# Optimization experiments

Hardware: AMD Instinct MI355X
Metric: run time of the kernel (lower is better)

The kernel has to match this reference:

```python
import jax, jax.numpy as jnp
import numpy as np

TOP_K = 15
TEMPERATURE = 1.0
NEG_SLOPE = 0.2


def setup_inputs() -> dict:
    key = jax.random.key(0)
    ks = jax.random.split(key, 6)
    N, H, heads, hd = 4096, 256, 4, 64
    E_c = 131072
    embeddings = jax.random.normal(ks[0], (N, H), dtype=jnp.float32)
    # nn.Linear(H, heads*hd, bias=False) weight: [heads*hd, H], xavier-ish scale
    W = jax.random.normal(ks[1], (heads * hd, H), dtype=jnp.float32) * (1.0 / np.sqrt(H))
    att = jax.random.normal(ks[2], (heads, 2 * hd), dtype=jnp.float32) * 0.1
    corr_lambda = jnp.ones((1,), dtype=jnp.float32)
    sector_mask = jax.random.uniform(ks[3], (N, N)) > 0.05
    active_mask = jnp.ones((N,), dtype=bool)
    corr_edge_index = jax.random.randint(ks[4], (2, E_c), 0, N)
    corr_edge_weight = jax.random.uniform(ks[5], (E_c,), minval=-1.0, maxval=1.0)
    return dict(embeddings=embeddings, W=W, att=att, corr_lambda=corr_lambda,
                sector_mask=sector_mask, active_mask=active_mask,
                corr_edge_index=corr_edge_index, corr_edge_weight=corr_edge_weight)


def reference(embeddings, W, att, corr_lambda, sector_mask, active_mask,
              corr_edge_index, corr_edge_weight):
    N = embeddings.shape[0]
    heads = att.shape[0]
    hd = att.shape[1] // 2
    # h: [N, heads, hd]
    h = (embeddings @ W.T).reshape(N, heads, hd)
    # algebraic split of concat([h_i || h_j]) . att  ->  s_dst[i] + s_src[j]
    a_dst, a_src = att[:, :hd], att[:, hd:]
    s_dst = jnp.einsum('nhd,hd->nh', h, a_dst)  # coefficient of row node i
    s_src = jnp.einsum('nhd,hd->nh', h, a_src)  # coefficient of col node j
    # [N, N, heads] broadcast-add, leaky_relu, mean over heads
    scores = jax.nn.leaky_relu(s_dst[:, None, :] + s_src[None, :, :], NEG_SLOPE)
    scores = scores.mean(axis=-1) / TEMPERATURE  # [N, N]
    mask = (active_mask[:, None] & active_mask[None, :]) & sector_mask  # [N, N]
    scores = jnp.where(mask, scores, -jnp.inf)
    # correlation prior scattered into a dense matrix (index-assign semantics)
    corr = jnp.zeros((N, N), dtype=scores.dtype).at[
        corr_edge_index[0], corr_edge_index[1]].set(corr_edge_weight.astype(scores.dtype))
    corr = corr * mask.astype(scores.dtype)
    scores = scores + corr_lambda[0] * corr
    k = min(TOP_K, N - 1)
    topk_scores, topk_idx = jax.lax.top_k(scores, k)  # per-row top-k over src dim
    rows = jnp.broadcast_to(jnp.arange(N)[:, None], (N, k))
    # dense mask guarantees all top-k entries are finite -> E = N*k fixed
    edge_index = jnp.stack([topk_idx.reshape(-1), rows.reshape(-1)], axis=0)  # [2, N*k]
    edge_weight = jax.nn.softmax(topk_scores, axis=1).reshape(-1)  # [N*k]
    return edge_index, edge_weight
```

## Files before the change

kernel.cpp:

```cpp
#include <hip/hip_runtime.h>
#include <math.h>

#define H_DIM 256
#define HEADS 4
#define HD 64
#define TOPK 15
#define NSLOPE 0.2
#define NSLOPEF 0.2f
#define EDGE_CAP_MAX 128
#define CAND_CAP 256

__global__ __launch_bounds__(256) void prep1_kernel(const float* __restrict__ W,
                                                    const float* __restrict__ att,
                                                    double* __restrict__ wa_dst,
                                                    double* __restrict__ wa_src,
                                                    int* __restrict__ cnt,
                                                    unsigned int* __restrict__ abits,
                                                    const int* __restrict__ active) {
    const int b = blockIdx.x;
    cnt[b * 256 + threadIdx.x] = 0;
    if (b < 2 * HEADS) {
        const int k = threadIdx.x;
        const int h = b >> 1;
        const int side = b & 1;
        double a = 0.0;
        for (int d = 0; d < HD; ++d)
            a += (double)W[(h * HD + d) * H_DIM + k] * (double)att[h * 2 * HD + side * HD + d];
        (side ? wa_src : wa_dst)[h * H_DIM + k] = a;
    } else if (b == 8 && threadIdx.x < 128) {
        const int* ap = active + threadIdx.x * 32;
        unsigned int wv = 0;
        for (int t = 0; t < 32; ++t)
            if (ap[t]) wv |= 1u << t;
        abits[threadIdx.x] = wv;
    }
}

__global__ __launch_bounds__(256) void prep2_kernel(
    const float* __restrict__ emb, const double* __restrict__ wa_dst,
    const double* __restrict__ wa_src, double* __restrict__ s_dst,
    double* __restrict__ s_src, float* __restrict__ s_dst_f,
    float* __restrict__ s_src_f, const int* __restrict__ eidx,
    const float* __restrict__ ew, int* __restrict__ cnt,
    int4* __restrict__ etab, int N, int E, int cap) {
    const int b = blockIdx.x;
    const int tid = threadIdx.x;

    if (b < 1024) {
        const int lane = tid & 63;
        const int wid = tid >> 6;
        const int i = b * 4 + wid;
        double e[4];
#pragma unroll
        for (int m = 0; m < 4; ++m) e[m] = (double)emb[(size_t)i * H_DIM + lane + 64 * m];
        double acc[8];
#pragma unroll
        for (int c = 0; c < 8; ++c) {
            const double* wa = (c & 1) ? wa_src : wa_dst;
            const int h = c >> 1;
            double a = 0.0;
#pragma unroll
            for (int m = 0; m < 4; ++m) a += e[m] * wa[h * H_DIM + lane + 64 * m];
            acc[c] = a;
        }
#pragma unroll
        for (int m = 1; m < 64; m <<= 1) {
#pragma unroll
            for (int c = 0; c < 8; ++c) acc[c] += __shfl_xor(acc[c], m, 64);
        }
        if (lane == 0) {
#pragma unroll
            for (int c = 0; c < 8; ++c) {
                const int h = c >> 1;
                if (c & 1) {
                    s_src[i * HEADS + h] = acc[c];
                    s_src_f[i * HEADS + h] = (float)acc[c];
                } else {
                    s_dst[i * HEADS + h] = acc[c];
                    s_dst_f[i * HEADS + h] = (float)acc[c];
                }
            }
        }
    } else {
        const int e = (b - 1024) * 256 + tid;
        if (e < E) {
            const int r = eidx[e];
            const int c = eidx[E + e];
            const int s = atomicAdd(&cnt[r], 1);
            if (s < cap) {
                int4 rec;
                rec.x = c;
                rec.y = e;
                rec.z = __float_as_int(ew[e]);
                rec.w = 0;
                etab[r * cap + s] = rec;
            }
        }
    }
}

#define FOR16(OP) OP(0) OP(1) OP(2) OP(3) OP(4) OP(5) OP(6) OP(7) \
                  OP(8) OP(9) OP(10) OP(11) OP(12) OP(13) OP(14) OP(15)

__global__ __launch_bounds__(256) void main_kernel(
    const double* __restrict__ s_dst, const double* __restrict__ s_src,
    const float* __restrict__ s_dst_f, const float* __restrict__ s_src_f,
    const int* __restrict__ sector_mask, const unsigned short* __restrict__ abits16,
    const int* __restrict__ active, const float* __restrict__ lam_p,
    const int* __restrict__ cnt, const int4* __restrict__ etab,
    float* __restrict__ out, int N, int cap) {
    const int i = blockIdx.x;
    const int tid = threadIdx.x;
    const int lane = tid & 63;
    const int wid = tid >> 6;

    __shared__ int ec[EDGE_CAP_MAX];
    __shared__ int ee[EDGE_CAP_MAX];
    __shared__ float ewl[EDGE_CAP_MAX];
    __shared__ int wcol[EDGE_CAP_MAX];
    __shared__ double wadd[EDGE_CAP_MAX];
    __shared__ unsigned int wth[4];
    __shared__ double cand_v[CAND_CAP];
    __shared__ int cand_i[CAND_CAP];
    __shared__ int cand_cnt, wcnt;
    __shared__ double sorted_v[TOPK];
    __shared__ int sorted_i[TOPK];
    __shared__ double exps[TOPK];

    if (tid == 0) { cand_cnt = 0; wcnt = 0; }

    int deg = cnt[i];
    if (deg > cap) deg = cap;
    for (int p = tid; p < deg; p += 256) {
        const int4 rec = etab[i * cap + p];
        ec[p] = rec.x;
        ee[p] = rec.y;
        ewl[p] = __int_as_float(rec.z);
    }
    __syncthreads();

    const int* mrow = sector_mask + (size_t)i * N;
    const int4 m0 = *(const int4*)(mrow + 16 * tid);
    const int4 m1 = *(const int4*)(mrow + 16 * tid + 4);
    const int4 m2 = *(const int4*)(mrow + 16 * tid + 8);
    const int4 m3 = *(const int4*)(mrow + 16 * tid + 12);
    const unsigned int act_us = (unsigned int)abits16[tid];
    unsigned int pb = 0;
#define PB(C, VAL) if ((VAL) != 0) pb |= (1u << (C));
    PB(0, m0.x)  PB(1, m0.y)  PB(2, m0.z)  PB(3, m0.w)
    PB(4, m1.x)  PB(5, m1.y)  PB(6, m1.z)  PB(7, m1.w)
    PB(8, m2.x)  PB(9, m2.y)  PB(10, m2.z) PB(11, m2.w)
    PB(12, m3.x) PB(13, m3.y) PB(14, m3.z) PB(15, m3.w)
#undef PB
    pb &= act_us;

    const int lhi = lane >> 4;
    const int llo = lane & 15;
    unsigned int pm = 0;
#pragma unroll
    for (int k = 0; k < 16; ++k) {
        const unsigned int opb = (unsigned int)__shfl((int)pb, 4 * k + lhi, 64);
        pm |= ((opb >> llo) & 1u) << k;
    }
    if (active[i] == 0) pm = 0;

    const float sdf0 = s_dst_f[i * 4 + 0];
    const float sdf1 = s_dst_f[i * 4 + 1];
    const float sdf2 = s_dst_f[i * 4 + 2];
    const float sdf3 = s_dst_f[i * 4 + 3];
    const double sd0 = s_dst[i * 4 + 0];
    const double sd1 = s_dst[i * 4 + 1];
    const double sd2 = s_dst[i * 4 + 2];
    const double sd3 = s_dst[i * 4 + 3];
    const double lam = (double)lam_p[0];
    const double4* __restrict__ s_src4 = (const double4*)s_src;
    const float4* __restrict__ s_srcf4 = (const float4*)s_src_f;
    const int jbase = (wid << 10) | lane;

    float f0, f1, f2, f3, f4, f5, f6, f7, f8, f9, f10, f11, f12, f13, f14, f15;
#define INIT_SLOT(K) { \
    const bool m = (pm >> K) & 1u; \
    const float4 sv = s_srcf4[jbase + (K << 6)]; \
    float x0 = sdf0 + sv.x, x1 = sdf1 + sv.y, x2 = sdf2 + sv.z, x3 = sdf3 + sv.w; \
    x0 = (x0 < 0.0f) ? NSLOPEF * x0 : x0; \
    x1 = (x1 < 0.0f) ? NSLOPEF * x1 : x1; \
    x2 = (x2 < 0.0f) ? NSLOPEF * x2 : x2; \
    x3 = (x3 < 0.0f) ? NSLOPEF * x3 : x3; \
    f##K = m ? (0.25f * (x0 + x1 + x2 + x3)) : -INFINITY; }
    FOR16(INIT_SLOT)
#undef INIT_SLOT

    if (tid < deg) {
        const int c = ec[tid];
        const int eid = ee[tid];
        bool win = true;
        for (int q = 0; q < deg; ++q)
            if (ec[q] == c && ee[q] > eid) win = false;
        if (win) {
            int p = atomicAdd(&wcnt, 1);
            wcol[p] = c;
            wadd[p] = lam * (double)ewl[tid];
        }
    }
    __syncthreads();

    const int nw = wcnt;
    for (int w = 0; w < nw; ++w) {
        const int c = wcol[w];
        if ((((c >> 10) << 6) | (c & 63)) == tid) {
            const float addf = (float)wadd[w];
            const int kk = (c >> 6) & 15;
#define ADD_SLOT(K) if (kk == K) f##K += addf;
            FOR16(ADD_SLOT)
#undef ADD_SLOT
        }
    }

    unsigned int k0, k1, k2, k3, k4, k5, k6, k7, k8, k9, k10, k11, k12, k13, k14, k15;
#define KEY_SLOT(K) { const unsigned u = __float_as_uint(f##K); \
    k##K = u ^ ((unsigned)((int)u >> 31) | 0x80000000u); }
    FOR16(KEY_SLOT)
#undef KEY_SLOT
    unsigned int lmax = k0;
#define LMAX(K) if (k##K > lmax) lmax = k##K;
    FOR16(LMAX)
#undef LMAX

    unsigned int th = 0;
    for (int b = 31; b >= 0; --b) {
        const unsigned int trial = th | (1u << b);
        unsigned long long m = __ballot(lmax >= trial);
        if (__popcll(m) >= TOPK) th = trial;
    }
    if (lane == 0) wth[wid] = th;
    __syncthreads();
    th = wth[0];
    if (wth[1] > th) th = wth[1];
    if (wth[2] > th) th = wth[2];
    if (wth[3] > th) th = wth[3];
    th = (th > 256u) ? (th - 256u) : 0u;

#define FILT(K) if (k##K >= th) { int p = atomicAdd(&cand_cnt, 1); \
    if (p < CAND_CAP) cand_i[p] = jbase + (K << 6); }
    FOR16(FILT)
#undef FILT
    __syncthreads();

    int C = cand_cnt;
    if (C > CAND_CAP) C = CAND_CAP;
    if (tid < C) {
        const int j = cand_i[tid];
        const double4 sv = s_src4[j];
        double x0 = sd0 + sv.x, x1 = sd1 + sv.y, x2 = sd2 + sv.z, x3 = sd3 + sv.w;
        x0 = (x0 < 0.0) ? NSLOPE * x0 : x0;
        x1 = (x1 < 0.0) ? NSLOPE * x1 : x1;
        x2 = (x2 < 0.0) ? NSLOPE * x2 : x2;
        x3 = (x3 < 0.0) ? NSLOPE * x3 : x3;
        double v = 0.25 * (x0 + x1 + x2 + x3);
        for (int w = 0; w < nw; ++w)
            if (wcol[w] == j) v += wadd[w];
        cand_v[tid] = v;
    }
    __syncthreads();

    if (tid < C) {
        const double mv = cand_v[tid];
        const int mi = cand_i[tid];
        int rank = 0;
        for (int q = 0; q < C; ++q) {
            const double qv = cand_v[q];
            const int qi = cand_i[q];
            rank += ((qv > mv) || (qv == mv && qi < mi)) ? 1 : 0;
        }
        if (rank < TOPK) { sorted_v[rank] = mv; sorted_i[rank] = mi; }
    }
    __syncthreads();

    if (tid < TOPK) exps[tid] = exp(sorted_v[tid] - sorted_v[0]);
    __syncthreads();
    if (tid < TOPK) {
        double s = 0.0;
        for (int t = 0; t < TOPK; ++t) s += exps[t];
        const int NK = N * TOPK;
        const int base = i * TOPK + tid;
        out[base] = (float)sorted_i[tid];
        out[NK + base] = (float)i;
        out[2 * NK + base] = (float)(exps[tid] / s);
    }
}

extern "C" void kernel_launch(void* const* d_in, const int* in_sizes, int n_in,
                              void* d_out, int out_size, void* d_ws, size_t ws_size,
                              hipStream_t stream) {
    const float* emb    = (const float*)d_in[0];
    const float* W      = (const float*)d_in[1];
    const float* att    = (const float*)d_in[2];
    const float* lam    = (const float*)d_in[3];
    const int*   sector = (const int*)d_in[4];
    const int*   active = (const int*)d_in[5];
    const int*   eidx   = (const int*)d_in[6];
    const float* ew     = (const float*)d_in[7];
    float* out = (float*)d_out;

    const int N = in_sizes[5];
    const int E = in_sizes[6] / 2;

    double* wa_dst = (double*)d_ws;
    double* wa_src = wa_dst + HEADS * H_DIM;
    double* s_dst  = wa_src + HEADS * H_DIM;
    double* s_src  = s_dst + (size_t)N * HEADS;
    float* s_dst_f = (float*)(s_src + (size_t)N * HEADS);
    float* s_src_f = s_dst_f + (size_t)N * HEADS;
    int* cnt       = (int*)(s_src_f + (size_t)N * HEADS);
    unsigned int* abits = (unsigned int*)(cnt + N);
    uintptr_t ep = (uintptr_t)(abits + N / 32);
    ep = (ep + 15) & ~(uintptr_t)15;
    int4* etab = (int4*)ep;

    size_t used = (ep - (uintptr_t)d_ws) + 64;
    size_t rem = (ws_size > used) ? (ws_size - used) : 0;
    int cap = (int)(rem / ((size_t)N * 16));
    if (cap > EDGE_CAP_MAX) cap = EDGE_CAP_MAX;
    if (cap < 16) cap = 16;

    const int nb = (E + 255) / 256;

    prep1_kernel<<<16, 256, 0, stream>>>(W, att, wa_dst, wa_src, cnt, abits, active);
    prep2_kernel<<<1024 + nb, 256, 0, stream>>>(emb, wa_dst, wa_src, s_dst, s_src,
                                                s_dst_f, s_src_f, eidx, ew, cnt,
                                                etab, N, E, cap);
    main_kernel<<<N, 256, 0, stream>>>(s_dst, s_src, s_dst_f, s_src_f, sector,
                                       (const unsigned short*)abits, active, lam, cnt,
                                       etab, out, N, cap);
}
```

Baseline: 179.6 us.

## Tile s_dst/s_src projection through shared memory, 16 rows per block

```diff
diff --git a/kernel.cpp b/kernel.cpp
--- a/kernel.cpp
+++ b/kernel.cpp
@@ -9,6 +9,7 @@
 #define NSLOPEF 0.2f
 #define EDGE_CAP_MAX 128
 #define CAND_CAP 256
+#define SROWS 16
 
 __global__ __launch_bounds__(256) void prep1_kernel(const float* __restrict__ W,
                                                     const float* __restrict__ att,
@@ -42,54 +43,55 @@
     double* __restrict__ s_src, float* __restrict__ s_dst_f,
     float* __restrict__ s_src_f, const int* __restrict__ eidx,
     const float* __restrict__ ew, int* __restrict__ cnt,
-    int4* __restrict__ etab, int N, int E, int cap) {
+    int4* __restrict__ etab, int N, int E, int cap, int sblocks) {
     const int b = blockIdx.x;
     const int tid = threadIdx.x;
 
-    if (b < 1024) {
-        const int lane = tid & 63;
-        const int wid = tid >> 6;
-        const int i = b * 4 + wid;
-        double e[4];
+    if (b < sblocks) {
+        __shared__ double wa_l[8][258];
+        __shared__ float emb_l[SROWS][258];
+        const int i0 = b * SROWS;
 #pragma unroll
-        for (int m = 0; m < 4; ++m) e[m] = (double)emb[(size_t)i * H_DIM + lane + 64 * m];
-        double acc[8];
+        for (int c = 0; c < 8; ++c)
+            wa_l[c][tid] = ((c & 1) ? wa_src : wa_dst)[(c >> 1) * H_DIM + tid];
 #pragma unroll
-        for (int c = 0; c < 8; ++c) {
-            const double* wa = (c & 1) ? wa_src : wa_dst;
+        for (int r = 0; r < SROWS; ++r)
+            emb_l[r][tid] = emb[(size_t)(i0 + r) * H_DIM + tid];
+        __syncthreads();
+
+        const int j = tid >> 1;
+        const int half = tid & 1;
+        const int r = j >> 3;
+        const int c = j & 7;
+        const int base = half * 128;
+        double acc = 0.0;
+#pragma unroll 8
+        for (int k = 0; k < 128; ++k)
+            acc += (double)emb_l[r][base + k] * wa_l[c][base + k];
+        const double other = __shfl_xor(acc, 1, 64);
+        const double lo = half ? other : acc;
+        const double hi = half ? acc : other;
+        const double s = lo + hi;
+        if (half == 0) {
+            const int i = i0 + r;
             const int h = c >> 1;
-            double a = 0.0;
-#pragma unroll
-            for (int m = 0; m < 4; ++m) a += e[m] * wa[h * H_DIM + lane + 64 * m];
-            acc[c] = a;
-        }
-#pragma unroll
-        for (int m = 1; m < 64; m <<= 1) {
-#pragma unroll
-            for (int c = 0; c < 8; ++c) acc[c] += __shfl_xor(acc[c], m, 64);
-        }
-        if (lane == 0) {
-#pragma unroll
-            for (int c = 0; c < 8; ++c) {
-                const int h = c >> 1;
-                if (c & 1) {
-                    s_src[i * HEADS + h] = acc[c];
-                    s_src_f[i * HEADS + h] = (float)acc[c];
-                } else {
-                    s_dst[i * HEADS + h] = acc[c];
-                    s_dst_f[i * HEADS + h] = (float)acc[c];
-                }
+            if (c & 1) {
+                s_src[i * HEADS + h] = s;
+                s_src_f[i * HEADS + h] = (float)s;
+            } else {
+                s_dst[i * HEADS + h] = s;
+                s_dst_f[i * HEADS + h] = (float)s;
             }
         }
     } else {
-        const int e = (b - 1024) * 256 + tid;
+        const int e = (b - sblocks) * 256 + tid;
         if (e < E) {
             const int r = eidx[e];
-            const int c = eidx[E + e];
+            const int cc = eidx[E + e];
             const int s = atomicAdd(&cnt[r], 1);
             if (s < cap) {
                 int4 rec;
-                rec.x = c;
+                rec.x = cc;
                 rec.y = e;
                 rec.z = __float_as_int(ew[e]);
                 rec.w = 0;
@@ -324,11 +326,12 @@
     if (cap < 16) cap = 16;
 
     const int nb = (E + 255) / 256;
+    const int sblocks = N / SROWS;
 
     prep1_kernel<<<16, 256, 0, stream>>>(W, att, wa_dst, wa_src, cnt, abits, active);
-    prep2_kernel<<<1024 + nb, 256, 0, stream>>>(emb, wa_dst, wa_src, s_dst, s_src,
-                                                s_dst_f, s_src_f, eidx, ew, cnt,
-                                                etab, N, E, cap);
+    prep2_kernel<<<sblocks + nb, 256, 0, stream>>>(emb, wa_dst, wa_src, s_dst, s_src,
+                                                   s_dst_f, s_src_f, eidx, ew, cnt,
+                                                   etab, N, E, cap, sblocks);
     main_kernel<<<N, 256, 0, stream>>>(s_dst, s_src, s_dst_f, s_src_f, sector,
                                        (const unsigned short*)abits, active, lam, cnt,
                                        etab, out, N, cap);
```

Result: no change. 177.9 us (-1.0%).
